# Performance work log

Measured on AMD Instinct MI355X. Metric: run time of the kernel, lower is better.

The kernel has to match this reference:

```python
import jax, jax.numpy as jnp
import numpy as np

DIAGNUM, MEDNUM, PRONUM, FEATDIM = 50000, 20000, 40000, 128
N1 = DIAGNUM + MEDNUM  # 70000
N2 = PRONUM + MEDNUM   # 60000
NNZ1, NNZ2 = 1_120_000, 960_000


def setup_inputs() -> dict:
    key = jax.random.key(0)
    ks = jax.random.split(key, 10)
    return {
        "adj1_rows": jax.random.randint(ks[0], (2, NNZ1), 0, N1, dtype=jnp.int32),
        "adj1_cols": jax.random.randint(ks[1], (2, NNZ1), 0, N1, dtype=jnp.int32),
        "adj1_vals": jax.random.uniform(ks[2], (2, NNZ1), dtype=jnp.float32),
        "adj2_rows": jax.random.randint(ks[3], (2, NNZ2), 0, N2, dtype=jnp.int32),
        "adj2_cols": jax.random.randint(ks[4], (2, NNZ2), 0, N2, dtype=jnp.int32),
        "adj2_vals": jax.random.uniform(ks[5], (2, NNZ2), dtype=jnp.float32),
        "dEmbed": jax.random.normal(ks[6], (DIAGNUM, FEATDIM), dtype=jnp.float32),
        "mEmbed": jax.random.normal(ks[7], (MEDNUM, FEATDIM), dtype=jnp.float32),
        "pEmbed": jax.random.normal(ks[8], (PRONUM, FEATDIM), dtype=jnp.float32),
        "inter": jax.random.uniform(ks[9], (1,), dtype=jnp.float32),
    }


def _spmm(rows, cols, vals, x, n):
    # sparse COO matmul: out[r] += vals * x[cols]
    msgs = vals[:, None] * x[cols]  # [nnz, d]
    return jax.ops.segment_sum(msgs, rows, num_segments=n)


def _gcn_layer(rows, cols, vals, x, n):
    h = _spmm(rows, cols, vals, x, n)
    h = jnp.where(h >= 0, h, 0.5 * h)  # LeakyReLU(0.5)
    return jax.nn.relu(h)              # extra F.relu in the loop


def reference(adj1_rows, adj1_cols, adj1_vals,
              adj2_rows, adj2_cols, adj2_vals,
              dEmbed, mEmbed, pEmbed, inter):
    diagnum, pronum = dEmbed.shape[0], pEmbed.shape[0]
    e1 = jnp.concatenate([dEmbed, mEmbed], axis=0)  # [N1, d]
    e2 = jnp.concatenate([pEmbed, mEmbed], axis=0)  # [N2, d]
    n1, n2 = e1.shape[0], e2.shape[0]
    # Original loops never extend lats1/lats2, so every iteration uses the
    # initial embeddings; each adj[i] contribution appears twice (j=0,1).
    g1 = jnp.zeros_like(e1)
    g2 = jnp.zeros_like(e2)
    for _j in range(2):
        for i in range(2):
            g1 = g1 + _gcn_layer(adj1_rows[i], adj1_cols[i], adj1_vals[i], e1, n1)
            g2 = g2 + _gcn_layer(adj2_rows[i], adj2_cols[i], adj2_vals[i], e2, n2)
    mEmbed_gcn_1 = g1[diagnum:]
    dEmbed_gcn = g1[:diagnum]
    mEmbed_gcn_2 = g2[pronum:]
    pEmbed_gcn = g2[:pronum]
    mEmbed_out = inter * mEmbed_gcn_1 + (1.0 - inter) * mEmbed_gcn_2
    return (mEmbed_out, dEmbed_gcn, pEmbed_gcn)
```

## Files before the change

kernel.cpp:

```cpp
#include <hip/hip_runtime.h>
#include <hip/hip_fp16.h>

#define DIAGNUM 50000
#define MEDNUM  20000
#define PRONUM  40000
#define FEATDIM 128
#define N1 (DIAGNUM + MEDNUM)
#define N2 (PRONUM + MEDNUM)
#define NNZ1 1120000
#define NNZ2 960000
#define NTOT (2 * N1 + 2 * N2)
#define NNZTOT (2 * NNZ1 + 2 * NNZ2)
#define NBUCK ((NTOT + 511) >> 9)
#define CAP 8704
#define L1_THREADS 512
#define L1_CHUNK 8192
#define L1_VITERS (L1_CHUNK / (L1_THREADS * 4))
#define L1_BLOCKS ((NNZTOT + L1_CHUNK - 1) / L1_CHUNK)

typedef unsigned short ushort_t;

__global__ __launch_bounds__(256) void init_cursor_kernel(int* __restrict__ cursor) {
    int b = blockIdx.x * 256 + threadIdx.x;
    if (b < NBUCK) cursor[b] = b * CAP;
}

__global__ __launch_bounds__(L1_THREADS) void lvl1_scatter_kernel(
        const int* __restrict__ a1r, const int* __restrict__ a1c,
        const float* __restrict__ a1v,
        const int* __restrict__ a2r, const int* __restrict__ a2c,
        const float* __restrict__ a2v,
        int* __restrict__ cursor, int2* __restrict__ lvl1) {
    __shared__ int lh[NBUCK];
    for (int b = threadIdx.x; b < NBUCK; b += L1_THREADS) lh[b] = 0;
    __syncthreads();
    int base = blockIdx.x * L1_CHUNK;
    int idxv[L1_VITERS * 4];
#pragma unroll
    for (int it = 0; it < L1_VITERS; it++) {
        int i = base + (it * L1_THREADS + threadIdx.x) * 4;
        if (i < NNZTOT) {
            int4 r4;
            int ofs;
            if (i < 2 * NNZ1) {
                r4 = *reinterpret_cast<const int4*>(a1r + i);
                ofs = (i < NNZ1) ? 0 : N1;
            } else {
                r4 = *reinterpret_cast<const int4*>(a2r + (i - 2 * NNZ1));
                ofs = 2 * N1 + ((i - 2 * NNZ1 < NNZ2) ? 0 : N2);
            }
            int idx0 = ofs + r4.x, idx1 = ofs + r4.y;
            int idx2 = ofs + r4.z, idx3 = ofs + r4.w;
            idxv[it * 4]     = idx0;
            idxv[it * 4 + 1] = idx1;
            idxv[it * 4 + 2] = idx2;
            idxv[it * 4 + 3] = idx3;
            atomicAdd(&lh[idx0 >> 9], 1);
            atomicAdd(&lh[idx1 >> 9], 1);
            atomicAdd(&lh[idx2 >> 9], 1);
            atomicAdd(&lh[idx3 >> 9], 1);
        }
    }
    __syncthreads();
    for (int b = threadIdx.x; b < NBUCK; b += L1_THREADS) {
        int h = lh[b];
        lh[b] = h ? atomicAdd(&cursor[b], h) : 0;
    }
    __syncthreads();
#pragma unroll
    for (int it = 0; it < L1_VITERS; it++) {
        int i = base + (it * L1_THREADS + threadIdx.x) * 4;
        if (i < NNZTOT) {
            int4 c4;
            float4 v4;
            if (i < 2 * NNZ1) {
                c4 = *reinterpret_cast<const int4*>(a1c + i);
                v4 = *reinterpret_cast<const float4*>(a1v + i);
            } else {
                c4 = *reinterpret_cast<const int4*>(a2c + (i - 2 * NNZ1));
                v4 = *reinterpret_cast<const float4*>(a2v + (i - 2 * NNZ1));
            }
            int idx0 = idxv[it * 4],     idx1 = idxv[it * 4 + 1];
            int idx2 = idxv[it * 4 + 2], idx3 = idxv[it * 4 + 3];
            int p0 = atomicAdd(&lh[idx0 >> 9], 1);
            lvl1[p0] = make_int2(((idx0 & 511) << 17) | c4.x, __float_as_int(v4.x));
            int p1 = atomicAdd(&lh[idx1 >> 9], 1);
            lvl1[p1] = make_int2(((idx1 & 511) << 17) | c4.y, __float_as_int(v4.y));
            int p2 = atomicAdd(&lh[idx2 >> 9], 1);
            lvl1[p2] = make_int2(((idx2 & 511) << 17) | c4.z, __float_as_int(v4.z));
            int p3 = atomicAdd(&lh[idx3 >> 9], 1);
            lvl1[p3] = make_int2(((idx3 & 511) << 17) | c4.w, __float_as_int(v4.w));
        }
    }
}

__global__ __launch_bounds__(512) void lvl2_sort_kernel(
        const int2* __restrict__ lvl1, const int* __restrict__ cursor,
        int* __restrict__ binned, int* __restrict__ rps, int* __restrict__ rpe) {
    extern __shared__ int2 lrec[];
    __shared__ int cnt[512];
    __shared__ int sc[512];
    int b = blockIdx.x;
    int t = threadIdx.x;
    int s0 = b * CAP;
    int e0 = cursor[b];
    int n  = e0 - s0;
    cnt[t] = 0;
    __syncthreads();
    for (int k = t; k < n; k += 512) {
        int2 rec = lvl1[s0 + k];
        lrec[k] = rec;
        atomicAdd(&cnt[rec.x >> 17], 1);
    }
    __syncthreads();
    int v = cnt[t];
    sc[t] = v;
    __syncthreads();
    for (int off = 1; off < 512; off <<= 1) {
        int y = (t >= off) ? sc[t - off] : 0;
        __syncthreads();
        sc[t] += y;
        __syncthreads();
    }
    int incl = sc[t];
    int excl = incl - v;
    int idx = (b << 9) + t;
    if (idx < NTOT) {
        rps[idx] = s0 + excl;
        rpe[idx] = s0 + incl;
    }
    cnt[t] = excl;
    __syncthreads();
    for (int k = t; k < n; k += 512) {
        int2 rec = lrec[k];
        int rl  = rec.x >> 17;
        int col = rec.x & 0x1FFFF;
        unsigned hv = __half_as_ushort(__float2half(__int_as_float(rec.y)));
        int pos = atomicAdd(&cnt[rl], 1);
        binned[s0 + pos] = (int)((hv << 17) | (unsigned)col);
    }
}

#define TOT8 ((DIAGNUM + MEDNUM + PRONUM) * (FEATDIM / 8))

__device__ __forceinline__ ushort_t f2h(float x) {
    return __half_as_ushort(__float2half(x));
}

__global__ __launch_bounds__(256) void convert_emb_kernel(
        const float* __restrict__ dE, const float* __restrict__ mE,
        const float* __restrict__ pE,
        ushort_t* __restrict__ emb1, ushort_t* __restrict__ emb2) {
    int t8 = blockIdx.x * 256 + threadIdx.x;
    if (t8 >= TOT8) return;
    long flat = (long)t8 * 8;
    const float* src;
    ushort_t* dst;
    ushort_t* dst2 = nullptr;
    if (flat < (long)DIAGNUM * FEATDIM) {
        src = dE + flat;
        dst = emb1 + flat;
    } else if (flat < (long)(DIAGNUM + MEDNUM) * FEATDIM) {
        long o = flat - (long)DIAGNUM * FEATDIM;
        src = mE + o;
        dst  = emb1 + (long)DIAGNUM * FEATDIM + o;
        dst2 = emb2 + (long)PRONUM * FEATDIM + o;
    } else {
        long o = flat - (long)(DIAGNUM + MEDNUM) * FEATDIM;
        src = pE + o;
        dst = emb2 + o;
    }
    float4 a = *reinterpret_cast<const float4*>(src);
    float4 b = *reinterpret_cast<const float4*>(src + 4);
    int4 w;
    w.x = (int)((unsigned)f2h(a.x) | ((unsigned)f2h(a.y) << 16));
    w.y = (int)((unsigned)f2h(a.z) | ((unsigned)f2h(a.w) << 16));
    w.z = (int)((unsigned)f2h(b.x) | ((unsigned)f2h(b.y) << 16));
    w.w = (int)((unsigned)f2h(b.z) | ((unsigned)f2h(b.w) << 16));
    *reinterpret_cast<int4*>(dst) = w;
    if (dst2) *reinterpret_cast<int4*>(dst2) = w;
}


__device__ __forceinline__ void fma8(float acc[8], float v, int4 h) {
    union U { int4 i; __half2 h2[4]; } u;
    u.i = h;
#pragma unroll
    for (int j = 0; j < 4; j++) {
        float2 f = __half22float2(u.h2[j]);
        acc[2 * j]     = fmaf(v, f.x, acc[2 * j]);
        acc[2 * j + 1] = fmaf(v, f.y, acc[2 * j + 1]);
    }
}

__device__ __forceinline__ float rec_val(unsigned rec) {
    return __half2float(__ushort_as_half((unsigned short)(rec >> 17)));
}

__device__ __forceinline__ void gather8(int s, int e,
                                        const int* __restrict__ binned,
                                        int q, int sub16,
                                        const ushort_t* __restrict__ emb,
                                        float acc[8]) {
    int k = s + q;
    for (; k + 4 < e; k += 8) {
        unsigned r0 = (unsigned)binned[k];
        unsigned r1 = (unsigned)binned[k + 4];
        const int4* b0 = reinterpret_cast<const int4*>(emb + ((size_t)(r0 & 0x1FFFFu) << 7));
        const int4* b1 = reinterpret_cast<const int4*>(emb + ((size_t)(r1 & 0x1FFFFu) << 7));
        int4 h0 = b0[sub16];
        int4 h1 = b1[sub16];
        fma8(acc, rec_val(r0), h0);
        fma8(acc, rec_val(r1), h1);
    }
    for (; k < e; k += 4) {
        unsigned r0 = (unsigned)binned[k];
        const int4* b0 = reinterpret_cast<const int4*>(emb + ((size_t)(r0 & 0x1FFFFu) << 7));
        int4 h0 = b0[sub16];
        fma8(acc, rec_val(r0), h0);
    }
}

__global__ __launch_bounds__(256) void fused_gcn_kernel(
        const int* __restrict__ rps, const int* __restrict__ rpe,
        const int* __restrict__ binned,
        const ushort_t* __restrict__ emb,
        const float* __restrict__ inter,
        float* __restrict__ out_d, float* __restrict__ out_p,
        float* __restrict__ out_m, int graph) {
    int gtid = blockIdx.x * blockDim.x + threadIdx.x;
    int w     = gtid >> 6;
    int lane  = gtid & 63;
    int q     = lane >> 4;
    int sub16 = lane & 15;

    int iA, iB, nrows;
    if (graph) { nrows = N1; iA = w;          iB = N1 + w; }
    else       { nrows = N2; iA = 2 * N1 + w; iB = 2 * N1 + N2 + w; }
    if (w >= nrows) return;

    float aA[8] = {0, 0, 0, 0, 0, 0, 0, 0};
    float aB[8] = {0, 0, 0, 0, 0, 0, 0, 0};
    gather8(rps[iA], rpe[iA], binned, q, sub16, emb, aA);
    gather8(rps[iB], rpe[iB], binned, q, sub16, emb, aB);

#pragma unroll
    for (int j = 0; j < 8; j++) {
        aA[j] += __shfl_xor(aA[j], 16);
        aA[j] += __shfl_xor(aA[j], 32);
        aB[j] += __shfl_xor(aB[j], 16);
        aB[j] += __shfl_xor(aB[j], 32);
    }

    if (lane >= 16) return;

    float r[8];
#pragma unroll
    for (int j = 0; j < 8; j++)
        r[j] = 2.f * (fmaxf(aA[j], 0.f) + fmaxf(aB[j], 0.f));

    float4 lo = make_float4(r[0], r[1], r[2], r[3]);
    float4 hi = make_float4(r[4], r[5], r[6], r[7]);

    if (graph) {
        if (w < DIAGNUM) {
            float4* dst = reinterpret_cast<float4*>(out_d + (size_t)w * FEATDIM);
            dst[sub16 * 2]     = lo;
            dst[sub16 * 2 + 1] = hi;
        } else {
            float t = *inter;
            float4* dst = reinterpret_cast<float4*>(
                out_m + (size_t)(w - DIAGNUM) * FEATDIM);
            float4 o0 = dst[sub16 * 2];
            float4 o1 = dst[sub16 * 2 + 1];
            o0.x = fmaf(t, lo.x, o0.x); o0.y = fmaf(t, lo.y, o0.y);
            o0.z = fmaf(t, lo.z, o0.z); o0.w = fmaf(t, lo.w, o0.w);
            o1.x = fmaf(t, hi.x, o1.x); o1.y = fmaf(t, hi.y, o1.y);
            o1.z = fmaf(t, hi.z, o1.z); o1.w = fmaf(t, hi.w, o1.w);
            dst[sub16 * 2]     = o0;
            dst[sub16 * 2 + 1] = o1;
        }
    } else {
        if (w < PRONUM) {
            float4* dst = reinterpret_cast<float4*>(out_p + (size_t)w * FEATDIM);
            dst[sub16 * 2]     = lo;
            dst[sub16 * 2 + 1] = hi;
        } else {
            float sc = 1.0f - *inter;
            lo.x *= sc; lo.y *= sc; lo.z *= sc; lo.w *= sc;
            hi.x *= sc; hi.y *= sc; hi.z *= sc; hi.w *= sc;
            float4* dst = reinterpret_cast<float4*>(
                out_m + (size_t)(w - PRONUM) * FEATDIM);
            dst[sub16 * 2]     = lo;
            dst[sub16 * 2 + 1] = hi;
        }
    }
}


extern "C" void kernel_launch(void* const* d_in, const int* in_sizes, int n_in,
                              void* d_out, int out_size, void* d_ws, size_t ws_size,
                              hipStream_t stream) {
    const int*   a1r = (const int*)d_in[0];
    const int*   a1c = (const int*)d_in[1];
    const float* a1v = (const float*)d_in[2];
    const int*   a2r = (const int*)d_in[3];
    const int*   a2c = (const int*)d_in[4];
    const float* a2v = (const float*)d_in[5];
    const float* dE  = (const float*)d_in[6];
    const float* mE  = (const float*)d_in[7];
    const float* pE  = (const float*)d_in[8];
    const float* inter = (const float*)d_in[9];

    float* out   = (float*)d_out;
    float* out_m = out;
    float* out_d = out + (size_t)MEDNUM * FEATDIM;
    float* out_p = out_d + (size_t)DIAGNUM * FEATDIM;

    char* ws = (char*)d_ws;
    int* binned = (int*)ws;          ws += (size_t)NBUCK * CAP * 4;
    char* regionB = ws;              ws += (size_t)NBUCK * CAP * 8;
    int2*     lvl1 = (int2*)regionB;
    ushort_t* emb1 = (ushort_t*)regionB;
    ushort_t* emb2 = emb1 + (size_t)N1 * FEATDIM;
    int* rps    = (int*)ws;          ws += (size_t)NTOT * 4;
    int* rpe    = (int*)ws;          ws += (size_t)NTOT * 4;
    int* cursor = (int*)ws;          ws += (size_t)NBUCK * 4;

    const int BLK = 256;

    init_cursor_kernel<<<(NBUCK + BLK - 1) / BLK, BLK, 0, stream>>>(cursor);
    lvl1_scatter_kernel<<<L1_BLOCKS, L1_THREADS, 0, stream>>>(
        a1r, a1c, a1v, a2r, a2c, a2v, cursor, lvl1);
    lvl2_sort_kernel<<<NBUCK, 512, (size_t)CAP * sizeof(int2), stream>>>(
        lvl1, cursor, binned, rps, rpe);

    convert_emb_kernel<<<(TOT8 + BLK - 1) / BLK, BLK, 0, stream>>>(
        dE, mE, pE, emb1, emb2);

    fused_gcn_kernel<<<(N2 + 3) / 4, BLK, 0, stream>>>(
        rps, rpe, binned, emb2, inter, out_d, out_p, out_m, 0);
    fused_gcn_kernel<<<(N1 + 3) / 4, BLK, 0, stream>>>(
        rps, rpe, binned, emb1, inter, out_d, out_p, out_m, 1);
}
```

Baseline: 216.2 us.

## Fuse embedding conversion into scatter kernel and merge both GCN launches

```diff
diff --git a/kernel.cpp b/kernel.cpp
--- a/kernel.cpp
+++ b/kernel.cpp
@@ -18,11 +18,62 @@
 #define L1_VITERS (L1_CHUNK / (L1_THREADS * 4))
 #define L1_BLOCKS ((NNZTOT + L1_CHUNK - 1) / L1_CHUNK)
 
+#define TOT8 ((DIAGNUM + MEDNUM + PRONUM) * (FEATDIM / 8))
+#define CONV_BLOCKS ((TOT8 + L1_THREADS - 1) / L1_THREADS)
+
+#define D_BLOCKS (DIAGNUM / 4)
+#define M_BLOCKS (MEDNUM / 4)
+#define P_BLOCKS (PRONUM / 4)
+
 typedef unsigned short ushort_t;
 
 __global__ __launch_bounds__(256) void init_cursor_kernel(int* __restrict__ cursor) {
     int b = blockIdx.x * 256 + threadIdx.x;
     if (b < NBUCK) cursor[b] = b * CAP;
+}
+
+__device__ __forceinline__ ushort_t f2h(float x) {
+    return __half_as_ushort(__float2half(x));
+}
+
+__device__ __forceinline__ void convert_t8(int t8,
+        const float* __restrict__ dE, const float* __restrict__ mE,
+        const float* __restrict__ pE,
+        ushort_t* __restrict__ emb1, ushort_t* __restrict__ emb2) {
+    long flat = (long)t8 * 8;
+    const float* src;
+    ushort_t* dst;
+    ushort_t* dst2 = nullptr;
+    if (flat < (long)DIAGNUM * FEATDIM) {
+        src = dE + flat;
+        dst = emb1 + flat;
+    } else if (flat < (long)(DIAGNUM + MEDNUM) * FEATDIM) {
+        long o = flat - (long)DIAGNUM * FEATDIM;
+        src = mE + o;
+        dst  = emb1 + (long)DIAGNUM * FEATDIM + o;
+        dst2 = emb2 + (long)PRONUM * FEATDIM + o;
+    } else {
+        long o = flat - (long)(DIAGNUM + MEDNUM) * FEATDIM;
+        src = pE + o;
+        dst = emb2 + o;
+    }
+    float4 a = *reinterpret_cast<const float4*>(src);
+    float4 b = *reinterpret_cast<const float4*>(src + 4);
+    int4 w;
+    w.x = (int)((unsigned)f2h(a.x) | ((unsigned)f2h(a.y) << 16));
+    w.y = (int)((unsigned)f2h(a.z) | ((unsigned)f2h(a.w) << 16));
+    w.z = (int)((unsigned)f2h(b.x) | ((unsigned)f2h(b.y) << 16));
+    w.w = (int)((unsigned)f2h(b.z) | ((unsigned)f2h(b.w) << 16));
+    *reinterpret_cast<int4*>(dst) = w;
+    if (dst2) *reinterpret_cast<int4*>(dst2) = w;
+}
+
+__global__ __launch_bounds__(256) void convert_emb_kernel(
+        const float* __restrict__ dE, const float* __restrict__ mE,
+        const float* __restrict__ pE,
+        ushort_t* __restrict__ emb1, ushort_t* __restrict__ emb2) {
+    int t8 = blockIdx.x * 256 + threadIdx.x;
+    if (t8 < TOT8) convert_t8(t8, dE, mE, pE, emb1, emb2);
 }
 
 __global__ __launch_bounds__(L1_THREADS) void lvl1_scatter_kernel(
@@ -30,7 +81,15 @@
         const float* __restrict__ a1v,
         const int* __restrict__ a2r, const int* __restrict__ a2c,
         const float* __restrict__ a2v,
-        int* __restrict__ cursor, int2* __restrict__ lvl1) {
+        int* __restrict__ cursor, int2* __restrict__ lvl1,
+        const float* __restrict__ dE, const float* __restrict__ mE,
+        const float* __restrict__ pE,
+        ushort_t* __restrict__ emb1, ushort_t* __restrict__ emb2) {
+    if (blockIdx.x >= L1_BLOCKS) {
+        int t8 = (blockIdx.x - L1_BLOCKS) * L1_THREADS + threadIdx.x;
+        if (t8 < TOT8) convert_t8(t8, dE, mE, pE, emb1, emb2);
+        return;
+    }
     __shared__ int lh[NBUCK];
     for (int b = threadIdx.x; b < NBUCK; b += L1_THREADS) lh[b] = 0;
     __syncthreads();
@@ -141,46 +200,6 @@
     }
 }
 
-#define TOT8 ((DIAGNUM + MEDNUM + PRONUM) * (FEATDIM / 8))
-
-__device__ __forceinline__ ushort_t f2h(float x) {
-    return __half_as_ushort(__float2half(x));
-}
-
-__global__ __launch_bounds__(256) void convert_emb_kernel(
-        const float* __restrict__ dE, const float* __restrict__ mE,
-        const float* __restrict__ pE,
-        ushort_t* __restrict__ emb1, ushort_t* __restrict__ emb2) {
-    int t8 = blockIdx.x * 256 + threadIdx.x;
-    if (t8 >= TOT8) return;
-    long flat = (long)t8 * 8;
-    const float* src;
-    ushort_t* dst;
-    ushort_t* dst2 = nullptr;
-    if (flat < (long)DIAGNUM * FEATDIM) {
-        src = dE + flat;
-        dst = emb1 + flat;
-    } else if (flat < (long)(DIAGNUM + MEDNUM) * FEATDIM) {
-        long o = flat - (long)DIAGNUM * FEATDIM;
-        src = mE + o;
-        dst  = emb1 + (long)DIAGNUM * FEATDIM + o;
-        dst2 = emb2 + (long)PRONUM * FEATDIM + o;
-    } else {
-        long o = flat - (long)(DIAGNUM + MEDNUM) * FEATDIM;
-        src = pE + o;
-        dst = emb2 + o;
-    }
-    float4 a = *reinterpret_cast<const float4*>(src);
-    float4 b = *reinterpret_cast<const float4*>(src + 4);
-    int4 w;
-    w.x = (int)((unsigned)f2h(a.x) | ((unsigned)f2h(a.y) << 16));
-    w.y = (int)((unsigned)f2h(a.z) | ((unsigned)f2h(a.w) << 16));
-    w.z = (int)((unsigned)f2h(b.x) | ((unsigned)f2h(b.y) << 16));
-    w.w = (int)((unsigned)f2h(b.z) | ((unsigned)f2h(b.w) << 16));
-    *reinterpret_cast<int4*>(dst) = w;
-    if (dst2) *reinterpret_cast<int4*>(dst2) = w;
-}
-
 
 __device__ __forceinline__ void fma8(float acc[8], float v, int4 h) {
     union U { int4 i; __half2 h2[4]; } u;
@@ -221,79 +240,71 @@
     }
 }
 
-__global__ __launch_bounds__(256) void fused_gcn_kernel(
-        const int* __restrict__ rps, const int* __restrict__ rpe,
-        const int* __restrict__ binned,
-        const ushort_t* __restrict__ emb,
-        const float* __restrict__ inter,
-        float* __restrict__ out_d, float* __restrict__ out_p,
-        float* __restrict__ out_m, int graph) {
-    int gtid = blockIdx.x * blockDim.x + threadIdx.x;
-    int w     = gtid >> 6;
-    int lane  = gtid & 63;
-    int q     = lane >> 4;
-    int sub16 = lane & 15;
-
-    int iA, iB, nrows;
-    if (graph) { nrows = N1; iA = w;          iB = N1 + w; }
-    else       { nrows = N2; iA = 2 * N1 + w; iB = 2 * N1 + N2 + w; }
-    if (w >= nrows) return;
-
+__device__ __forceinline__ void row_pair(int iA, int iB,
+                                         const int* __restrict__ rps,
+                                         const int* __restrict__ rpe,
+                                         const int* __restrict__ binned,
+                                         int q, int sub16,
+                                         const ushort_t* __restrict__ emb,
+                                         float r[8]) {
     float aA[8] = {0, 0, 0, 0, 0, 0, 0, 0};
     float aB[8] = {0, 0, 0, 0, 0, 0, 0, 0};
     gather8(rps[iA], rpe[iA], binned, q, sub16, emb, aA);
     gather8(rps[iB], rpe[iB], binned, q, sub16, emb, aB);
-
 #pragma unroll
     for (int j = 0; j < 8; j++) {
         aA[j] += __shfl_xor(aA[j], 16);
         aA[j] += __shfl_xor(aA[j], 32);
         aB[j] += __shfl_xor(aB[j], 16);
         aB[j] += __shfl_xor(aB[j], 32);
-    }
-
-    if (lane >= 16) return;
-
-    float r[8];
-#pragma unroll
-    for (int j = 0; j < 8; j++)
         r[j] = 2.f * (fmaxf(aA[j], 0.f) + fmaxf(aB[j], 0.f));
-
-    float4 lo = make_float4(r[0], r[1], r[2], r[3]);
-    float4 hi = make_float4(r[4], r[5], r[6], r[7]);
-
-    if (graph) {
-        if (w < DIAGNUM) {
-            float4* dst = reinterpret_cast<float4*>(out_d + (size_t)w * FEATDIM);
-            dst[sub16 * 2]     = lo;
-            dst[sub16 * 2 + 1] = hi;
-        } else {
-            float t = *inter;
-            float4* dst = reinterpret_cast<float4*>(
-                out_m + (size_t)(w - DIAGNUM) * FEATDIM);
-            float4 o0 = dst[sub16 * 2];
-            float4 o1 = dst[sub16 * 2 + 1];
-            o0.x = fmaf(t, lo.x, o0.x); o0.y = fmaf(t, lo.y, o0.y);
-            o0.z = fmaf(t, lo.z, o0.z); o0.w = fmaf(t, lo.w, o0.w);
-            o1.x = fmaf(t, hi.x, o1.x); o1.y = fmaf(t, hi.y, o1.y);
-            o1.z = fmaf(t, hi.z, o1.z); o1.w = fmaf(t, hi.w, o1.w);
-            dst[sub16 * 2]     = o0;
-            dst[sub16 * 2 + 1] = o1;
-        }
+    }
+}
+
+__global__ __launch_bounds__(256) void fused_gcn_kernel(
+        const int* __restrict__ rps, const int* __restrict__ rpe,
+        const int* __restrict__ binned,
+        const ushort_t* __restrict__ emb1, const ushort_t* __restrict__ emb2,
+        const float* __restrict__ inter,
+        float* __restrict__ out_d, float* __restrict__ out_p,
+        float* __restrict__ out_m) {
+    int bid   = blockIdx.x;
+    int wv    = threadIdx.x >> 6;
+    int lane  = threadIdx.x & 63;
+    int q     = lane >> 4;
+    int sub16 = lane & 15;
+
+    if (bid < D_BLOCKS) {
+        int r = bid * 4 + wv;
+        float res[8];
+        row_pair(r, N1 + r, rps, rpe, binned, q, sub16, emb1, res);
+        if (lane >= 16) return;
+        float4* dst = reinterpret_cast<float4*>(out_d + (size_t)r * FEATDIM);
+        dst[sub16 * 2]     = make_float4(res[0], res[1], res[2], res[3]);
+        dst[sub16 * 2 + 1] = make_float4(res[4], res[5], res[6], res[7]);
+    } else if (bid < D_BLOCKS + M_BLOCKS) {
+        int m = (bid - D_BLOCKS) * 4 + wv;
+        float r1[8], r2[8];
+        row_pair(DIAGNUM + m, N1 + DIAGNUM + m, rps, rpe, binned, q, sub16, emb1, r1);
+        row_pair(2 * N1 + PRONUM + m, 2 * N1 + N2 + PRONUM + m,
+                 rps, rpe, binned, q, sub16, emb2, r2);
+        if (lane >= 16) return;
+        float t = *inter;
+        float res[8];
+#pragma unroll
+        for (int j = 0; j < 8; j++)
+            res[j] = fmaf(t, r1[j] - r2[j], r2[j]);
+        float4* dst = reinterpret_cast<float4*>(out_m + (size_t)m * FEATDIM);
+        dst[sub16 * 2]     = make_float4(res[0], res[1], res[2], res[3]);
+        dst[sub16 * 2 + 1] = make_float4(res[4], res[5], res[6], res[7]);
     } else {
-        if (w < PRONUM) {
-            float4* dst = reinterpret_cast<float4*>(out_p + (size_t)w * FEATDIM);
-            dst[sub16 * 2]     = lo;
-            dst[sub16 * 2 + 1] = hi;
-        } else {
-            float sc = 1.0f - *inter;
-            lo.x *= sc; lo.y *= sc; lo.z *= sc; lo.w *= sc;
-            hi.x *= sc; hi.y *= sc; hi.z *= sc; hi.w *= sc;
-            float4* dst = reinterpret_cast<float4*>(
-                out_m + (size_t)(w - PRONUM) * FEATDIM);
-            dst[sub16 * 2]     = lo;
-            dst[sub16 * 2 + 1] = hi;
-        }
+        int r = (bid - D_BLOCKS - M_BLOCKS) * 4 + wv;
+        float res[8];
+        row_pair(2 * N1 + r, 2 * N1 + N2 + r, rps, rpe, binned, q, sub16, emb2, res);
+        if (lane >= 16) return;
+        float4* dst = reinterpret_cast<float4*>(out_p + (size_t)r * FEATDIM);
+        dst[sub16 * 2]     = make_float4(res[0], res[1], res[2], res[3]);
+        dst[sub16 * 2 + 1] = make_float4(res[4], res[5], res[6], res[7]);
     }
 }
 
@@ -317,29 +328,48 @@
     float* out_d = out + (size_t)MEDNUM * FEATDIM;
     float* out_p = out_d + (size_t)DIAGNUM * FEATDIM;
 
+    const size_t SZ_BINNED = (size_t)NBUCK * CAP * 4;
+    const size_t SZ_LVL1   = (size_t)NBUCK * CAP * 8;
+    const size_t SZ_EMB    = (size_t)(N1 + N2) * FEATDIM * 2;
+    const size_t SZ_MISC   = (size_t)NTOT * 8 + (size_t)NBUCK * 4 + 64;
+
+    const int BLK = 256;
+
     char* ws = (char*)d_ws;
-    int* binned = (int*)ws;          ws += (size_t)NBUCK * CAP * 4;
-    char* regionB = ws;              ws += (size_t)NBUCK * CAP * 8;
-    int2*     lvl1 = (int2*)regionB;
-    ushort_t* emb1 = (ushort_t*)regionB;
+    int* binned = (int*)ws;          ws += SZ_BINNED;
+
+    bool bigws = ws_size >= SZ_BINNED + SZ_LVL1 + SZ_EMB + SZ_MISC;
+
+    int2*     lvl1;
+    ushort_t* emb1;
+    if (bigws) {
+        lvl1 = (int2*)ws;            ws += SZ_LVL1;
+        emb1 = (ushort_t*)ws;        ws += SZ_EMB;
+    } else {
+        lvl1 = (int2*)ws;
+        emb1 = (ushort_t*)ws;        ws += SZ_LVL1;
+    }
     ushort_t* emb2 = emb1 + (size_t)N1 * FEATDIM;
     int* rps    = (int*)ws;          ws += (size_t)NTOT * 4;
     int* rpe    = (int*)ws;          ws += (size_t)NTOT * 4;
     int* cursor = (int*)ws;          ws += (size_t)NBUCK * 4;
 
-    const int BLK = 256;
-
     init_cursor_kernel<<<(NBUCK + BLK - 1) / BLK, BLK, 0, stream>>>(cursor);
-    lvl1_scatter_kernel<<<L1_BLOCKS, L1_THREADS, 0, stream>>>(
-        a1r, a1c, a1v, a2r, a2c, a2v, cursor, lvl1);
-    lvl2_sort_kernel<<<NBUCK, 512, (size_t)CAP * sizeof(int2), stream>>>(
-        lvl1, cursor, binned, rps, rpe);
-
-    convert_emb_kernel<<<(TOT8 + BLK - 1) / BLK, BLK, 0, stream>>>(
-        dE, mE, pE, emb1, emb2);
-
-    fused_gcn_kernel<<<(N2 + 3) / 4, BLK, 0, stream>>>(
-        rps, rpe, binned, emb2, inter, out_d, out_p, out_m, 0);
-    fused_gcn_kernel<<<(N1 + 3) / 4, BLK, 0, stream>>>(
-        rps, rpe, binned, emb1, inter, out_d, out_p, out_m, 1);
-}
+
+    if (bigws) {
+        lvl1_scatter_kernel<<<L1_BLOCKS + CONV_BLOCKS, L1_THREADS, 0, stream>>>(
+            a1r, a1c, a1v, a2r, a2c, a2v, cursor, lvl1, dE, mE, pE, emb1, emb2);
+        lvl2_sort_kernel<<<NBUCK, 512, (size_t)CAP * sizeof(int2), stream>>>(
+            lvl1, cursor, binned, rps, rpe);
+    } else {
+        lvl1_scatter_kernel<<<L1_BLOCKS, L1_THREADS, 0, stream>>>(
+            a1r, a1c, a1v, a2r, a2c, a2v, cursor, lvl1, dE, mE, pE, emb1, emb2);
+        lvl2_sort_kernel<<<NBUCK, 512, (size_t)CAP * sizeof(int2), stream>>>(
+            lvl1, cursor, binned, rps, rpe);
+        convert_emb_kernel<<<(TOT8 + BLK - 1) / BLK, BLK, 0, stream>>>(
+            dE, mE, pE, emb1, emb2);
+    }
+
+    fused_gcn_kernel<<<D_BLOCKS + M_BLOCKS + P_BLOCKS, BLK, 0, stream>>>(
+        rps, rpe, binned, emb1, emb2, inter, out_d, out_p, out_m);
+}
```

Measured after the change: 229.6 us. +6.2%, slower.

## Fuse embedding fp16 conversion into bucket sort and replace cursor init with memset

Applied to the files above, without the earlier changes.

```diff
diff --git a/kernel.cpp b/kernel.cpp
--- a/kernel.cpp
+++ b/kernel.cpp
@@ -18,19 +18,17 @@
 #define L1_VITERS (L1_CHUNK / (L1_THREADS * 4))
 #define L1_BLOCKS ((NNZTOT + L1_CHUNK - 1) / L1_CHUNK)
 
+#define CONV4_PER_BLK (CAP / 2)
+#define EMB_TOT4 ((N1 + N2) * (FEATDIM / 8))
+
 typedef unsigned short ushort_t;
-
-__global__ __launch_bounds__(256) void init_cursor_kernel(int* __restrict__ cursor) {
-    int b = blockIdx.x * 256 + threadIdx.x;
-    if (b < NBUCK) cursor[b] = b * CAP;
-}
 
 __global__ __launch_bounds__(L1_THREADS) void lvl1_scatter_kernel(
         const int* __restrict__ a1r, const int* __restrict__ a1c,
         const float* __restrict__ a1v,
         const int* __restrict__ a2r, const int* __restrict__ a2c,
         const float* __restrict__ a2v,
-        int* __restrict__ cursor, int2* __restrict__ lvl1) {
+        int* __restrict__ czero, int2* __restrict__ lvl1) {
     __shared__ int lh[NBUCK];
     for (int b = threadIdx.x; b < NBUCK; b += L1_THREADS) lh[b] = 0;
     __syncthreads();
@@ -64,7 +62,7 @@
     __syncthreads();
     for (int b = threadIdx.x; b < NBUCK; b += L1_THREADS) {
         int h = lh[b];
-        lh[b] = h ? atomicAdd(&cursor[b], h) : 0;
+        lh[b] = h ? (b * CAP + atomicAdd(&czero[b], h)) : 0;
     }
     __syncthreads();
 #pragma unroll
@@ -94,16 +92,22 @@
     }
 }
 
+__device__ __forceinline__ ushort_t f2h(float x) {
+    return __half_as_ushort(__float2half(x));
+}
+
 __global__ __launch_bounds__(512) void lvl2_sort_kernel(
-        const int2* __restrict__ lvl1, const int* __restrict__ cursor,
-        int* __restrict__ binned, int* __restrict__ rps, int* __restrict__ rpe) {
+        const int2* __restrict__ lvl1, const int* __restrict__ czero,
+        int* __restrict__ binned, int* __restrict__ rps, int* __restrict__ rpe,
+        const float* __restrict__ dE, const float* __restrict__ mE,
+        const float* __restrict__ pE, int4* __restrict__ embOut) {
     extern __shared__ int2 lrec[];
     __shared__ int cnt[512];
     __shared__ int sc[512];
     int b = blockIdx.x;
     int t = threadIdx.x;
     int s0 = b * CAP;
-    int e0 = cursor[b];
+    int e0 = s0 + czero[b];
     int n  = e0 - s0;
     cnt[t] = 0;
     __syncthreads();
@@ -139,46 +143,23 @@
         int pos = atomicAdd(&cnt[rl], 1);
         binned[s0 + pos] = (int)((hv << 17) | (unsigned)col);
     }
-}
-
-#define TOT8 ((DIAGNUM + MEDNUM + PRONUM) * (FEATDIM / 8))
-
-__device__ __forceinline__ ushort_t f2h(float x) {
-    return __half_as_ushort(__float2half(x));
-}
-
-__global__ __launch_bounds__(256) void convert_emb_kernel(
-        const float* __restrict__ dE, const float* __restrict__ mE,
-        const float* __restrict__ pE,
-        ushort_t* __restrict__ emb1, ushort_t* __restrict__ emb2) {
-    int t8 = blockIdx.x * 256 + threadIdx.x;
-    if (t8 >= TOT8) return;
-    long flat = (long)t8 * 8;
-    const float* src;
-    ushort_t* dst;
-    ushort_t* dst2 = nullptr;
-    if (flat < (long)DIAGNUM * FEATDIM) {
-        src = dE + flat;
-        dst = emb1 + flat;
-    } else if (flat < (long)(DIAGNUM + MEDNUM) * FEATDIM) {
-        long o = flat - (long)DIAGNUM * FEATDIM;
-        src = mE + o;
-        dst  = emb1 + (long)DIAGNUM * FEATDIM + o;
-        dst2 = emb2 + (long)PRONUM * FEATDIM + o;
-    } else {
-        long o = flat - (long)(DIAGNUM + MEDNUM) * FEATDIM;
-        src = pE + o;
-        dst = emb2 + o;
-    }
-    float4 a = *reinterpret_cast<const float4*>(src);
-    float4 b = *reinterpret_cast<const float4*>(src + 4);
-    int4 w;
-    w.x = (int)((unsigned)f2h(a.x) | ((unsigned)f2h(a.y) << 16));
-    w.y = (int)((unsigned)f2h(a.z) | ((unsigned)f2h(a.w) << 16));
-    w.z = (int)((unsigned)f2h(b.x) | ((unsigned)f2h(b.y) << 16));
-    w.w = (int)((unsigned)f2h(b.z) | ((unsigned)f2h(b.w) << 16));
-    *reinterpret_cast<int4*>(dst) = w;
-    if (dst2) *reinterpret_cast<int4*>(dst2) = w;
+    int u4end = min((b + 1) * CONV4_PER_BLK, EMB_TOT4);
+    for (int u4 = b * CONV4_PER_BLK + t; u4 < u4end; u4 += 512) {
+        int g = u4 * 8;
+        const float* src;
+        if (g < DIAGNUM * FEATDIM)            src = dE + g;
+        else if (g < N1 * FEATDIM)            src = mE + (g - DIAGNUM * FEATDIM);
+        else if (g < (N1 + PRONUM) * FEATDIM) src = pE + (g - N1 * FEATDIM);
+        else                                  src = mE + (g - (N1 + PRONUM) * FEATDIM);
+        float4 a = *reinterpret_cast<const float4*>(src);
+        float4 c = *reinterpret_cast<const float4*>(src + 4);
+        int4 w;
+        w.x = (int)((unsigned)f2h(a.x) | ((unsigned)f2h(a.y) << 16));
+        w.y = (int)((unsigned)f2h(a.z) | ((unsigned)f2h(a.w) << 16));
+        w.z = (int)((unsigned)f2h(c.x) | ((unsigned)f2h(c.y) << 16));
+        w.w = (int)((unsigned)f2h(c.z) | ((unsigned)f2h(c.w) << 16));
+        embOut[u4] = w;
+    }
 }
 
 
@@ -325,18 +306,15 @@
     ushort_t* emb2 = emb1 + (size_t)N1 * FEATDIM;
     int* rps    = (int*)ws;          ws += (size_t)NTOT * 4;
     int* rpe    = (int*)ws;          ws += (size_t)NTOT * 4;
-    int* cursor = (int*)ws;          ws += (size_t)NBUCK * 4;
+    int* czero  = (int*)ws;          ws += (size_t)NBUCK * 4;
 
     const int BLK = 256;
 
-    init_cursor_kernel<<<(NBUCK + BLK - 1) / BLK, BLK, 0, stream>>>(cursor);
+    (void)hipMemsetAsync(czero, 0, (size_t)NBUCK * sizeof(int), stream);
     lvl1_scatter_kernel<<<L1_BLOCKS, L1_THREADS, 0, stream>>>(
-        a1r, a1c, a1v, a2r, a2c, a2v, cursor, lvl1);
+        a1r, a1c, a1v, a2r, a2c, a2v, czero, lvl1);
     lvl2_sort_kernel<<<NBUCK, 512, (size_t)CAP * sizeof(int2), stream>>>(
-        lvl1, cursor, binned, rps, rpe);
-
-    convert_emb_kernel<<<(TOT8 + BLK - 1) / BLK, BLK, 0, stream>>>(
-        dE, mE, pE, emb1, emb2);
+        lvl1, czero, binned, rps, rpe, dE, mE, pE, (int4*)regionB);
 
     fused_gcn_kernel<<<(N2 + 3) / 4, BLK, 0, stream>>>(
         rps, rpe, binned, emb2, inter, out_d, out_p, out_m, 0);
```

Measured after the change: 228.2 us. 5.5% more time.
